# Performance work log

Measured on AMD Instinct MI355X. Metric: run time of the kernel, lower is better.

The kernel has to match this reference:

```python
import jax, jax.numpy as jnp
import numpy as np

B, S, C = 256, 169, 512      # batch, input seq_len (hardcoded 169 in source), n_attn
H, TT, HS = 256, 256, 16     # n_head, ctx_len, head_size (all forced by hardcoded shapes)
OUT = 64                     # output Linear(16, 64)


def setup_inputs() -> dict:
    key = jax.random.key(0)
    ks = jax.random.split(key, 13)
    s_in = 1.0 / np.sqrt(C)
    s_hs = 1.0 / np.sqrt(HS)
    return {
        "x": jax.random.normal(ks[0], (B, S, C), dtype=jnp.float32),
        "time_w": jax.random.normal(ks[1], (H, TT), dtype=jnp.float32) * 0.1,
        "time_alpha": jax.random.normal(ks[2], (H, 1, TT), dtype=jnp.float32) * 0.1 + 1.0,
        "time_beta": jax.random.normal(ks[3], (H, TT, 1), dtype=jnp.float32) * 0.1 + 1.0,
        "time_gamma": jax.random.normal(ks[4], (TT, 1), dtype=jnp.float32) * 0.1 + 1.0,
        "key_w": jax.random.normal(ks[5], (HS, C), dtype=jnp.float32) * s_in,
        "key_b": jax.random.normal(ks[6], (HS,), dtype=jnp.float32) * s_in,
        "value_w": jax.random.normal(ks[7], (HS, C), dtype=jnp.float32) * s_in,
        "value_b": jax.random.normal(ks[8], (HS,), dtype=jnp.float32) * s_in,
        "recep_w": jax.random.normal(ks[9], (HS, C), dtype=jnp.float32) * s_in,
        "recep_b": jax.random.normal(ks[10], (HS,), dtype=jnp.float32) * s_in,
        "out_w": jax.random.normal(ks[11], (OUT, HS), dtype=jnp.float32) * s_hs,
        "out_b": jax.random.normal(ks[12], (OUT,), dtype=jnp.float32) * s_hs,
    }


def reference(x, time_w, time_alpha, time_beta, time_gamma,
              key_w, key_b, value_w, value_b, recep_w, recep_b,
              out_w, out_b):
    # --- build the time-decay matrix via the pad/tile shift trick ---
    w = jnp.pad(time_w, ((0, 0), (0, TT)))            # (H, 2TT)
    w = jnp.tile(w, (1, TT))                          # (H, 2TT*TT)
    w = w[:, :-TT].reshape(H, TT, 2 * TT - 1)
    w = w[:, :, TT - 1:]                              # (H, TT, TT)
    w = w * time_alpha * time_beta                    # (H, TT, TT)

    # --- channel-half time shift: first C/2 channels shifted back by 1 step ---
    half = C // 2
    shifted = jnp.pad(x[:, :, :half], ((0, 0), (1, 0), (0, 0)))[:, :-1]
    x = jnp.concatenate([shifted, x[:, :, half:]], axis=-1)

    # --- projections (torch Linear: y = x @ W.T + b) ---
    k = x @ key_w.T + key_b                           # (B, S, HS)
    v = x @ value_w.T + value_b
    r = x @ recep_w.T + recep_b

    pad_len = TT - S                                  # 256 - 169 = 87
    r = jnp.pad(r, ((0, 0), (0, pad_len), (0, 0)))    # (B, TT, HS)

    k = jnp.exp(jnp.clip(k, -60.0, 30.0))
    sum_k = jnp.cumsum(k, axis=1)                     # (B, S, HS)
    sum_k = jnp.pad(sum_k, ((0, 0), (0, pad_len), (0, 0)))  # (B, TT, HS)

    kv = k * v                                        # (B, S, HS)
    kv = jnp.pad(kv, ((0, 0), (0, pad_len), (0, 0)))  # (B, TT, HS)

    # einsum('htu,bhc->btc') == contract u first, then (t,h) matmul against kv's seq axis
    w2 = w.sum(axis=-1)                               # (H, TT): sum_u w[h,t,u]
    wkv = jnp.einsum('ht,bhc->btc', w2, kv)           # (B, TT, HS)

    # original divides by zero-padded sum_k in the padded tail; guard with 1 there
    denom = jnp.where(sum_k == 0, jnp.ones_like(sum_k), sum_k)
    rwkv = jax.nn.sigmoid(r) * wkv / denom            # (B, TT, HS)

    rwkv = rwkv @ out_w.T + out_b                     # (B, TT, 64)
    rwkv = rwkv * time_gamma[:TT]                     # (TT,1) broadcast
    return rwkv
```

## Files before the change

### kernel.cpp

```cpp
#include <hip/hip_runtime.h>

typedef unsigned short u16;
typedef unsigned int u32;
typedef __attribute__((ext_vector_type(8))) __bf16 bf16x8;
typedef __attribute__((ext_vector_type(4))) float f32x4;

#define S_LEN 169
#define C_DIM 512
#define SP 192

#define WT_OFF  0
#define XT0_OFF 49152
#define XT1_OFF 71680
#define KE_OFF  0
#define KVF_OFF 11264
#define RF_OFF  22528
#define KVT_OFF 33792
#define G_OFF   39936
#define RB_OFF  51200
#define SS_OFF  71680
#define OW_OFF  72704
#define LDS_BYTES 94208

__global__ __launch_bounds__(1024) void w2_kernel(
    const float* __restrict__ time_w,
    const float* __restrict__ time_alpha,
    const float* __restrict__ time_beta,
    __bf16* __restrict__ w2t)
{
    __shared__ float tw[256];
    __shared__ float al[256];
    __shared__ float part[4][256];
    const int s = blockIdx.x;
    const int t = threadIdx.x & 255;
    const int p = threadIdx.x >> 8;
    if (s >= S_LEN) {
        if (p == 0) w2t[t * SP + s] = (__bf16)0.f;
        return;
    }
    if (p == 0) { tw[t] = time_w[s * 256 + t]; al[t] = time_alpha[s * 256 + t]; }
    __syncthreads();
    const int u0 = p << 6;
    const int u1 = (u0 + 64 < t + 1) ? (u0 + 64) : (t + 1);
    float acc = 0.f;
    for (int u = u0; u < u1; ++u)
        acc = fmaf(tw[255 + u - t], al[u], acc);
    part[p][t] = acc;
    __syncthreads();
    if (p == 0)
        w2t[t * SP + s] = (__bf16)(time_beta[s * 256 + t] *
                                   (part[0][t] + part[1][t] + part[2][t] + part[3][t]));
}

__global__ __launch_bounds__(512) void rwkv_main(
    const float* __restrict__ x,
    const float* __restrict__ key_w, const float* __restrict__ key_b,
    const float* __restrict__ value_w, const float* __restrict__ value_b,
    const float* __restrict__ recep_w, const float* __restrict__ recep_b,
    const float* __restrict__ out_w, const float* __restrict__ out_b,
    const float* __restrict__ gamma,
    const __bf16* __restrict__ w2t,
    float* __restrict__ out)
{
    __shared__ __align__(16) char smem[LDS_BYTES];
    const int tid  = threadIdx.x;
    const int lane = tid & 63;
    const int wid  = tid >> 6;
    const int q    = lane >> 4;
    const int hs   = lane & 15;
    const int b    = blockIdx.x;
    const float* xb = x + (size_t)b * (S_LEN * C_DIM);

    for (int i = tid; i < 3072; i += 512) {
        int j  = i >> 6;
        int co = (i & 63) << 3;
        const float* src;
        if (j < 16)      src = key_w   + j * 512 + co;
        else if (j < 32) src = value_w + (j - 16) * 512 + co;
        else             src = recep_w + (j - 32) * 512 + co;
        float4 f0 = *(const float4*)src;
        float4 f1 = *(const float4*)(src + 4);
        bf16x8 p;
        p[0]=(__bf16)f0.x; p[1]=(__bf16)f0.y; p[2]=(__bf16)f0.z; p[3]=(__bf16)f0.w;
        p[4]=(__bf16)f1.x; p[5]=(__bf16)f1.y; p[6]=(__bf16)f1.z; p[7]=(__bf16)f1.w;
        u32 off = (((u32)j << 10) + ((u32)co << 1)) ^ (((u32)(j & 7)) << 4);
        *(bf16x8*)(smem + WT_OFF + off) = p;
    }

    const float kb = key_b[hs];
    const float vb = value_b[hs];
    const float rb = recep_b[hs];

    f32x4 acc0[3], acc1[3];
    #pragma unroll
    for (int n = 0; n < 3; ++n) { acc0[n] = (f32x4){0.f,0.f,0.f,0.f}; acc1[n] = (f32x4){0.f,0.f,0.f,0.f}; }
    const bool has_m1 = (wid < 3);

    float4 pf[3][2];
    int pv[3];

    auto ldchunk = [&](int chunk) {
        const bool shifted = chunk < 4;
        #pragma unroll
        for (int it = 0; it < 3; ++it) {
            int i = tid + (it << 9);
            pv[it] = 0;
            if (i < 1408) {
                int r = i >> 3;
                int tsrc = shifted ? (r - 1) : r;
                bool valid = shifted ? (r >= 1 && r <= S_LEN) : (r < S_LEN);
                pv[it] = 1;
                if (valid) {
                    const float* src = xb + (size_t)tsrc * C_DIM + (chunk << 6) + ((i & 7) << 3);
                    pf[it][0] = *(const float4*)src;
                    pf[it][1] = *(const float4*)(src + 4);
                    pv[it] = 2;
                }
            }
        }
    };

    auto cvtwrite = [&](u32 base) {
        #pragma unroll
        for (int it = 0; it < 3; ++it) {
            int i = tid + (it << 9);
            if (i < 1408 && pv[it]) {
                int r = i >> 3, co = (i & 7) << 3;
                bf16x8 p = {(__bf16)0.f,(__bf16)0.f,(__bf16)0.f,(__bf16)0.f,
                            (__bf16)0.f,(__bf16)0.f,(__bf16)0.f,(__bf16)0.f};
                if (pv[it] == 2) {
                    p[0]=(__bf16)pf[it][0].x; p[1]=(__bf16)pf[it][0].y;
                    p[2]=(__bf16)pf[it][0].z; p[3]=(__bf16)pf[it][0].w;
                    p[4]=(__bf16)pf[it][1].x; p[5]=(__bf16)pf[it][1].y;
                    p[6]=(__bf16)pf[it][1].z; p[7]=(__bf16)pf[it][1].w;
                }
                u32 off = (((u32)r << 7) + ((u32)co << 1)) ^ (((u32)(r & 7)) << 4);
                *(bf16x8*)(smem + base + off) = p;
            }
        }
    };

    auto mfma_chunk = [&](int chunk, u32 xbase) {
        #pragma unroll
        for (int ks = 0; ks < 2; ++ks) {
            int kc = ks << 5;
            bf16x8 bfr[3];
            #pragma unroll
            for (int nt = 0; nt < 3; ++nt) {
                int j = nt * 16 + hs;
                u32 col = (u32)((chunk << 6) + kc + (q << 3));
                u32 off = (((u32)j << 10) + (col << 1)) ^ (((u32)(j & 7)) << 4);
                bfr[nt] = *(const bf16x8*)(smem + WT_OFF + off);
            }
            {
                int row = wid * 16 + hs;
                u32 off = (((u32)row << 7) + ((u32)(kc + (q << 3)) << 1)) ^ (((u32)(row & 7)) << 4);
                bf16x8 afr = *(const bf16x8*)(smem + xbase + off);
                acc0[0] = __builtin_amdgcn_mfma_f32_16x16x32_bf16(afr, bfr[0], acc0[0], 0,0,0);
                acc0[1] = __builtin_amdgcn_mfma_f32_16x16x32_bf16(afr, bfr[1], acc0[1], 0,0,0);
                acc0[2] = __builtin_amdgcn_mfma_f32_16x16x32_bf16(afr, bfr[2], acc0[2], 0,0,0);
            }
            if (has_m1) {
                int row = (wid + 8) * 16 + hs;
                u32 off = (((u32)row << 7) + ((u32)(kc + (q << 3)) << 1)) ^ (((u32)(row & 7)) << 4);
                bf16x8 afr = *(const bf16x8*)(smem + xbase + off);
                acc1[0] = __builtin_amdgcn_mfma_f32_16x16x32_bf16(afr, bfr[0], acc1[0], 0,0,0);
                acc1[1] = __builtin_amdgcn_mfma_f32_16x16x32_bf16(afr, bfr[1], acc1[1], 0,0,0);
                acc1[2] = __builtin_amdgcn_mfma_f32_16x16x32_bf16(afr, bfr[2], acc1[2], 0,0,0);
            }
        }
    };

    ldchunk(0);
    cvtwrite(XT0_OFF);
    __syncthreads();
    #pragma unroll
    for (int chunk = 0; chunk < 8; ++chunk) {
        const u32 cur = (chunk & 1) ? XT1_OFF : XT0_OFF;
        const u32 nxt = (chunk & 1) ? XT0_OFF : XT1_OFF;
        if (chunk < 7) ldchunk(chunk + 1);
        mfma_chunk(chunk, cur);
        if (chunk < 7) cvtwrite(nxt);
        __syncthreads();
    }

    float* kef = (float*)(smem + KE_OFF);
    float* kvf = (float*)(smem + KVF_OFF);
    float* rff = (float*)(smem + RF_OFF);
    #pragma unroll
    for (int m = 0; m < 2; ++m) {
        if (m == 1 && !has_m1) break;
        const f32x4* A = (m == 0) ? acc0 : acc1;
        int tb = (wid + m * 8) * 16 + (q << 2);
        float ke[4];
        #pragma unroll
        for (int rg = 0; rg < 4; ++rg) {
            float kk = A[0][rg] + kb;
            kk = fminf(fmaxf(kk, -60.f), 30.f);
            ke[rg] = __expf(kk);
        }
        #pragma unroll
        for (int rg = 0; rg < 4; ++rg) {
            int t = tb + rg;
            kef[t * 16 + hs] = ke[rg];
            kvf[t * 16 + hs] = ke[rg] * (A[1][rg] + vb);
            rff[t * 16 + hs] = A[2][rg] + rb;
        }
    }
    __syncthreads();

    float* seg = (float*)(smem + SS_OFF);
    float* g   = (float*)(smem + G_OFF);
    if (tid < 256) {
        int h = tid & 15, sg = tid >> 4;
        int t0 = sg * 11, t1 = (t0 + 11 < S_LEN) ? t0 + 11 : S_LEN;
        float s = 0.f;
        for (int t = t0; t < t1; ++t) s += kef[t * 16 + h];
        seg[sg * 16 + h] = s;
    } else {
        int i2 = tid - 256;
        for (int i = i2; i < 4096; i += 256) {
            int row = i >> 4, c = 16 + (i & 15);
            ((__bf16*)(smem + RB_OFF))[row * 40 + c] = (__bf16)0.f;
        }
        for (int i = i2; i < 368; i += 256) {
            int h = i & 15; int t = S_LEN + (i >> 4);
            u32 off = ((u32)(h * 384 + t * 2)) ^ (((u32)(h & 7)) << 4);
            *(__bf16*)(smem + KVT_OFF + off) = (__bf16)0.f;
        }
        for (int i = i2; i < 2560; i += 256) {
            int o = i / 40, c = i - o * 40;
            ((__bf16*)(smem + OW_OFF))[o * 40 + c] = (c < 16) ? (__bf16)out_w[o * 16 + c] : (__bf16)0.f;
        }
    }
    __syncthreads();
    if (tid < 16) {
        float run = 0.f;
        for (int sg = 0; sg < 16; ++sg) {
            float v = seg[sg * 16 + tid];
            seg[sg * 16 + tid] = run;
            run += v;
        }
    }
    __syncthreads();
    if (tid < 256) {
        int h = tid & 15, sg = tid >> 4;
        int t0 = sg * 11, t1 = (t0 + 11 < S_LEN) ? t0 + 11 : S_LEN;
        float run = seg[sg * 16 + h];
        for (int t = t0; t < t1; ++t) {
            run += kef[t * 16 + h];
            u32 off = ((u32)(h * 384 + t * 2)) ^ (((u32)(h & 7)) << 4);
            *(__bf16*)(smem + KVT_OFF + off) = (__bf16)kvf[t * 16 + h];
            float rr = rff[t * 16 + h];
            float sig = 1.f / (1.f + __expf(-rr));
            g[t * 16 + h] = sig / run;
        }
    }
    __syncthreads();

    f32x4 wa0 = (f32x4){0.f,0.f,0.f,0.f};
    f32x4 wa1 = (f32x4){0.f,0.f,0.f,0.f};
    #pragma unroll
    for (int s0 = 0; s0 < SP; s0 += 32) {
        int scol = s0 + (q << 3);
        u32 boff = ((u32)(hs * 384 + scol * 2)) ^ (((u32)(hs & 7)) << 4);
        bf16x8 bfr = *(const bf16x8*)(smem + KVT_OFF + boff);
        {
            int row = wid * 16 + hs;
            bf16x8 afr = *(const bf16x8*)(w2t + row * SP + scol);
            wa0 = __builtin_amdgcn_mfma_f32_16x16x32_bf16(afr, bfr, wa0, 0,0,0);
        }
        {
            int row = (wid + 8) * 16 + hs;
            bf16x8 afr = *(const bf16x8*)(w2t + row * SP + scol);
            wa1 = __builtin_amdgcn_mfma_f32_16x16x32_bf16(afr, bfr, wa1, 0,0,0);
        }
    }
    #pragma unroll
    for (int m = 0; m < 2; ++m) {
        const f32x4& W = (m == 0) ? wa0 : wa1;
        int tb = (wid + m * 8) * 16 + (q << 2);
        #pragma unroll
        for (int rg = 0; rg < 4; ++rg) {
            int t = tb + rg;
            float fac = (t < S_LEN) ? g[t * 16 + hs] : 0.5f;
            ((__bf16*)(smem + RB_OFF))[t * 40 + hs] = (__bf16)(W[rg] * fac);
        }
    }
    __syncthreads();

    float obv[4];
    #pragma unroll
    for (int nt = 0; nt < 4; ++nt) obv[nt] = out_b[nt * 16 + hs];
    #pragma unroll
    for (int m = 0; m < 2; ++m) {
        int mt = wid + m * 8;
        int arow = mt * 16 + hs;
        bf16x8 afr = *(const bf16x8*)(smem + RB_OFF + (u32)(arow * 80 + (q << 4)));
        float gm[4];
        #pragma unroll
        for (int rg = 0; rg < 4; ++rg) gm[rg] = gamma[mt * 16 + (q << 2) + rg];
        #pragma unroll
        for (int nt = 0; nt < 4; ++nt) {
            int orow = nt * 16 + hs;
            bf16x8 bfr = *(const bf16x8*)(smem + OW_OFF + (u32)(orow * 80 + (q << 4)));
            f32x4 zc = (f32x4){0.f,0.f,0.f,0.f};
            f32x4 d = __builtin_amdgcn_mfma_f32_16x16x32_bf16(afr, bfr, zc, 0,0,0);
            #pragma unroll
            for (int rg = 0; rg < 4; ++rg) {
                int t = mt * 16 + (q << 2) + rg;
                out[(size_t)b * 16384 + (size_t)t * 64 + nt * 16 + hs] = (d[rg] + obv[nt]) * gm[rg];
            }
        }
    }
}

extern "C" void kernel_launch(void* const* d_in, const int* in_sizes, int n_in,
                              void* d_out, int out_size, void* d_ws, size_t ws_size,
                              hipStream_t stream) {
    const float* x          = (const float*)d_in[0];
    const float* time_w     = (const float*)d_in[1];
    const float* time_alpha = (const float*)d_in[2];
    const float* time_beta  = (const float*)d_in[3];
    const float* time_gamma = (const float*)d_in[4];
    const float* key_w      = (const float*)d_in[5];
    const float* key_b      = (const float*)d_in[6];
    const float* value_w    = (const float*)d_in[7];
    const float* value_b    = (const float*)d_in[8];
    const float* recep_w    = (const float*)d_in[9];
    const float* recep_b    = (const float*)d_in[10];
    const float* out_w      = (const float*)d_in[11];
    const float* out_b      = (const float*)d_in[12];
    __bf16* w2t = (__bf16*)d_ws;

    w2_kernel<<<192, 1024, 0, stream>>>(time_w, time_alpha, time_beta, w2t);
    rwkv_main<<<256, 512, 0, stream>>>(x, key_w, key_b, value_w, value_b,
                                       recep_w, recep_b, out_w, out_b,
                                       time_gamma, w2t, (float*)d_out);
}
```

Baseline: 38.12 us.

## Prefetch x chunks two ahead with split register buffers and lgkm-only barriers

Loads of x chunks are now issued two iterations ahead, using two alternating register buffer sets, so global-load latency overlaps more MFMA work. __syncthreads is replaced by an asm s_waitcnt lgkmcnt(0) plus s_barrier, which waits only on LDS traffic and not on outstanding global loads. The serial 16-thread segment prefix scan and its barrier are removed; each thread instead sums the preceding segments itself, and the sigmoid/divide pair is merged into one reciprocal. This raises register pressure (two prefetch buffers) and depends on the hand-written barrier being correct with respect to outstanding vmem loads.

After: 38.06 us. Within noise of the previous version (-0.2%).

```diff
diff --git a/kernel.cpp b/kernel.cpp
--- a/kernel.cpp
+++ b/kernel.cpp
@@ -21,6 +21,8 @@
 #define SS_OFF  71680
 #define OW_OFF  72704
 #define LDS_BYTES 94208
+
+#define LGKM_BAR() asm volatile("s_waitcnt lgkmcnt(0)\n\ts_barrier" ::: "memory")
 
 __global__ __launch_bounds__(1024) void w2_kernel(
     const float* __restrict__ time_w,
@@ -96,10 +98,10 @@
     for (int n = 0; n < 3; ++n) { acc0[n] = (f32x4){0.f,0.f,0.f,0.f}; acc1[n] = (f32x4){0.f,0.f,0.f,0.f}; }
     const bool has_m1 = (wid < 3);
 
-    float4 pf[3][2];
-    int pv[3];
-
-    auto ldchunk = [&](int chunk) {
+    float4 pfA[3][2]; int pvA[3];
+    float4 pfB[3][2]; int pvB[3];
+
+    auto ldchunk = [&](int chunk, float4 (&pf)[3][2], int (&pv)[3]) {
         const bool shifted = chunk < 4;
         #pragma unroll
         for (int it = 0; it < 3; ++it) {
@@ -120,7 +122,7 @@
         }
     };
 
-    auto cvtwrite = [&](u32 base) {
+    auto cvtwrite = [&](u32 base, float4 (&pf)[3][2], int (&pv)[3]) {
         #pragma unroll
         for (int it = 0; it < 3; ++it) {
             int i = tid + (it << 9);
@@ -171,17 +173,26 @@
         }
     };
 
-    ldchunk(0);
-    cvtwrite(XT0_OFF);
-    __syncthreads();
+    ldchunk(0, pfA, pvA);
+    cvtwrite(XT0_OFF, pfA, pvA);
+    ldchunk(1, pfA, pvA);
+    ldchunk(2, pfB, pvB);
+    LGKM_BAR();
+
     #pragma unroll
     for (int chunk = 0; chunk < 8; ++chunk) {
         const u32 cur = (chunk & 1) ? XT1_OFF : XT0_OFF;
         const u32 nxt = (chunk & 1) ? XT0_OFF : XT1_OFF;
-        if (chunk < 7) ldchunk(chunk + 1);
         mfma_chunk(chunk, cur);
-        if (chunk < 7) cvtwrite(nxt);
-        __syncthreads();
+        if (chunk < 7) {
+            if (chunk & 1) cvtwrite(nxt, pfB, pvB);
+            else           cvtwrite(nxt, pfA, pvA);
+        }
+        LGKM_BAR();
+        if (chunk < 5) {
+            if (chunk & 1) ldchunk(chunk + 3, pfB, pvB);
+            else           ldchunk(chunk + 3, pfA, pvA);
+        }
     }
 
     float* kef = (float*)(smem + KE_OFF);
@@ -224,8 +235,8 @@
             ((__bf16*)(smem + RB_OFF))[row * 40 + c] = (__bf16)0.f;
         }
         for (int i = i2; i < 368; i += 256) {
-            int h = i & 15; int t = S_LEN + (i >> 4);
-            u32 off = ((u32)(h * 384 + t * 2)) ^ (((u32)(h & 7)) << 4);
+            int h2 = i & 15; int t = S_LEN + (i >> 4);
+            u32 off = ((u32)(h2 * 384 + t * 2)) ^ (((u32)(h2 & 7)) << 4);
             *(__bf16*)(smem + KVT_OFF + off) = (__bf16)0.f;
         }
         for (int i = i2; i < 2560; i += 256) {
@@ -234,26 +245,18 @@
         }
     }
     __syncthreads();
-    if (tid < 16) {
-        float run = 0.f;
-        for (int sg = 0; sg < 16; ++sg) {
-            float v = seg[sg * 16 + tid];
-            seg[sg * 16 + tid] = run;
-            run += v;
-        }
-    }
-    __syncthreads();
+
     if (tid < 256) {
         int h = tid & 15, sg = tid >> 4;
+        float run = 0.f;
+        for (int s2 = 0; s2 < sg; ++s2) run += seg[s2 * 16 + h];
         int t0 = sg * 11, t1 = (t0 + 11 < S_LEN) ? t0 + 11 : S_LEN;
-        float run = seg[sg * 16 + h];
         for (int t = t0; t < t1; ++t) {
             run += kef[t * 16 + h];
             u32 off = ((u32)(h * 384 + t * 2)) ^ (((u32)(h & 7)) << 4);
             *(__bf16*)(smem + KVT_OFF + off) = (__bf16)kvf[t * 16 + h];
             float rr = rff[t * 16 + h];
-            float sig = 1.f / (1.f + __expf(-rr));
-            g[t * 16 + h] = sig / run;
+            g[t * 16 + h] = 1.f / ((1.f + __expf(-rr)) * run);
         }
     }
     __syncthreads();
```
